# Performance work log

Hardware: AMD Instinct MI355X
Metric: run time of the kernel (lower is better)

## Reference

```python
import jax, jax.numpy as jnp
import numpy as np

B, S, C, H = 8, 1024, 512, 8
DH = C // H  # channels per head


def setup_inputs() -> dict:
    key = jax.random.key(0)
    ks = jax.random.split(key, 10)
    s = 1.0 / np.sqrt(C)
    return {
        "pe_lin_encoding": jax.random.normal(ks[0], (B, S, C), jnp.float32),
        "pe_lin_skip": jax.random.normal(ks[1], (B, S, C), jnp.float32),
        "Wq": jax.random.normal(ks[2], (C, C), jnp.float32) * s,
        "bq": jax.random.normal(ks[3], (C,), jnp.float32) * s,
        "Wk": jax.random.normal(ks[4], (C, C), jnp.float32) * s,
        "bk": jax.random.normal(ks[5], (C,), jnp.float32) * s,
        "Wv": jax.random.normal(ks[6], (C, C), jnp.float32) * s,
        "bv": jax.random.normal(ks[7], (C,), jnp.float32) * s,
        "Wo": jax.random.normal(ks[8], (C, C), jnp.float32) * s,
        "bo": jax.random.normal(ks[9], (C,), jnp.float32) * s,
    }


def reference(pe_lin_encoding, pe_lin_skip, Wq, bq, Wk, bk, Wv, bv, Wo, bo):
    # flatten trailing dims (already [B, S, C] here)
    x = pe_lin_encoding.reshape(pe_lin_encoding.shape[0], pe_lin_encoding.shape[1], -1)
    # torch Linear convention: y = x @ W^T + b, W is [out, in]
    q = jnp.einsum("bsc,oc->bso", x, Wq) + bq
    k = jnp.einsum("bsc,oc->bso", x, Wk) + bk
    v = jnp.einsum("bsc,oc->bso", x, Wv) + bv
    # split heads: [B, S, H, DH] -> attention per head
    q = q.reshape(B, S, H, DH)
    k = k.reshape(B, S, H, DH)
    v = v.reshape(B, S, H, DH)
    scale = 1.0 / np.sqrt(DH)
    scores = jnp.einsum("bqhd,bkhd->bhqk", q, k) * scale  # [B,H,S,S]
    attn = jax.nn.softmax(scores, axis=-1)
    ctx = jnp.einsum("bhqk,bkhd->bqhd", attn, v).reshape(B, S, C)
    out = jnp.einsum("bsc,oc->bso", ctx, Wo) + bo
    return out + pe_lin_skip
```

## Files before the change

### kernel.cpp

```cpp
#include <hip/hip_runtime.h>
#include <hip/hip_bf16.h>

typedef unsigned short u16;
typedef unsigned int u32;

constexpr int B  = 8;
constexpr int S  = 1024;
constexpr int C  = 512;
constexpr int H  = 8;
constexpr int DH = 64;
constexpr int M  = B * S;

typedef __attribute__((ext_vector_type(8))) short bf16x8;
typedef __attribute__((ext_vector_type(4))) float f32x4;

#define GLOBAL_AS __attribute__((address_space(1)))
#define LDS_AS    __attribute__((address_space(3)))

#define QSCALE 0.1803368867f

__device__ __forceinline__ float bf2f(u16 u) {
    return __uint_as_float(((u32)u) << 16);
}
__device__ __forceinline__ u16 f2bf(float f) {
    u32 u = __float_as_uint(f);
    u += 0x7fffu + ((u >> 16) & 1u);
    return (u16)(u >> 16);
}
__device__ __forceinline__ u32 pack2(float a, float b) {
    return (u32)f2bf(a) | ((u32)f2bf(b) << 16);
}
__device__ __forceinline__ void async_cp16(const u16* g, u16* l) {
    __builtin_amdgcn_global_load_lds((const GLOBAL_AS void*)g, (LDS_AS void*)l, 16, 0, 0);
}

constexpr int NX4 = M * C / 4;
constexpr int NW4 = C * C / 4;

__global__ __launch_bounds__(256) void cvt_kernel(
    const float* __restrict__ x,
    const float* __restrict__ wq, const float* __restrict__ wk,
    const float* __restrict__ wv, const float* __restrict__ wo,
    u16* __restrict__ xb, u16* __restrict__ wqkv, u16* __restrict__ wob)
{
    const int i = blockIdx.x * 256 + threadIdx.x;
    const float* src; u16* dst; int off;
    if      (i < NX4)          { src = x;  dst = xb;           off = i; }
    else if (i < NX4 +   NW4)  { src = wq; dst = wqkv;         off = i - NX4; }
    else if (i < NX4 + 2*NW4)  { src = wk; dst = wqkv + C*C;   off = i - NX4 -   NW4; }
    else if (i < NX4 + 3*NW4)  { src = wv; dst = wqkv + 2*C*C; off = i - NX4 - 2*NW4; }
    else                       { src = wo; dst = wob;          off = i - NX4 - 3*NW4; }
    float4 v = ((const float4*)src)[off];
    uint2 p; p.x = pack2(v.x, v.y); p.y = pack2(v.z, v.w);
    ((uint2*)dst)[off] = p;
}

__global__ __launch_bounds__(256) void qkv_gemm(
    const u16* __restrict__ xb, const u16* __restrict__ wqkv,
    const float* __restrict__ bq, const float* __restrict__ bk,
    const float* __restrict__ bv,
    u16* __restrict__ Qo, u16* __restrict__ Ko, u16* __restrict__ Vo)
{
    __shared__ alignas(16) u16 smem[128 * 136];
    u16* const Asm = smem;
    u16* const Bsm = smem + 128 * 64;

    const int mTile = blockIdx.x * 128;
    const int nTile = blockIdx.y * 128;
    const int t = threadIdx.x, lane = t & 63, w = t >> 6;
    const int ql = lane & 15, quad = lane >> 4;
    const int wm = (w & 1) * 64, wn = (w >> 1) * 64;

    f32x4 acc[4][4];
    #pragma unroll
    for (int i = 0; i < 4; i++)
        #pragma unroll
        for (int j = 0; j < 4; j++) acc[i][j] = (f32x4){0.f, 0.f, 0.f, 0.f};

    for (int k0 = 0; k0 < C; k0 += 64) {
        __syncthreads();
        #pragma unroll
        for (int q = 0; q < 4; q++) {
            const int chunk = q * 256 + t;
            const int row = chunk >> 3, c8 = (chunk & 7) * 8;
            async_cp16(xb   + (size_t)(mTile + row) * C + k0 + c8, &Asm[row * 64 + c8]);
            async_cp16(wqkv + (size_t)(nTile + row) * C + k0 + c8, &Bsm[row * 64 + c8]);
        }
        __syncthreads();

        #pragma unroll
        for (int ks = 0; ks < 64; ks += 32) {
            bf16x8 af[4], bfr[4];
            #pragma unroll
            for (int i = 0; i < 4; i++)
                af[i] = *(const bf16x8*)&Asm[(wm + i*16 + ql) * 64 + ks + quad*8];
            #pragma unroll
            for (int j = 0; j < 4; j++)
                bfr[j] = *(const bf16x8*)&Bsm[(wn + j*16 + ql) * 64 + ks + quad*8];
            #pragma unroll
            for (int i = 0; i < 4; i++)
                #pragma unroll
                for (int j = 0; j < 4; j++)
                    acc[i][j] = __builtin_amdgcn_mfma_f32_16x16x32_bf16(af[i], bfr[j], acc[i][j], 0, 0, 0);
        }
    }

    const int z = nTile >> 9;
    const int nBase = nTile & 511;
    if (z == 2) {
        __syncthreads();
        u16* const T = smem;
        #pragma unroll
        for (int j = 0; j < 4; j++) {
            const int n = wn + j*16 + ql;
            const float bj = bv[nBase + n];
            #pragma unroll
            for (int i = 0; i < 4; i++)
                #pragma unroll
                for (int r = 0; r < 4; r++)
                    T[n * 136 + wm + i*16 + quad*4 + r] = f2bf(acc[i][j][r] + bj);
        }
        __syncthreads();
        const int bb = mTile >> 10, ssBase = mTile & 1023;
        #pragma unroll
        for (int q = 0; q < 8; q++) {
            const int c = q * 256 + t;
            const int row = c >> 4, col = (c & 15) * 8;
            const int o = nBase + row, h = o >> 6, d = o & 63;
            *(float4*)(Vo + ((size_t)((bb*H + h) * DH + d)) * S + ssBase + col) =
                *(const float4*)&T[row * 136 + col];
        }
    } else {
        const float* bias = (z == 0) ? bq : bk;
        u16* dst          = (z == 0) ? Qo : Ko;
        const float sc    = (z == 0) ? QSCALE : 1.0f;
        #pragma unroll
        for (int j = 0; j < 4; j++) {
            const int o = nBase + wn + j*16 + ql;
            const float bj = bias[o];
            const int h = o >> 6, d = o & 63;
            #pragma unroll
            for (int i = 0; i < 4; i++) {
                #pragma unroll
                for (int r = 0; r < 4; r++) {
                    const int m = mTile + wm + i*16 + quad*4 + r;
                    const int bb = m >> 10, ss = m & 1023;
                    dst[(size_t)((bb*H + h) * S + ss) * DH + d] = f2bf((acc[i][j][r] + bj) * sc);
                }
            }
        }
    }
}

__global__ __launch_bounds__(256) void attn_kernel(
    const u16* __restrict__ Qo,
    const u16* __restrict__ Ko,
    const u16* __restrict__ Vo,
    u16* __restrict__ ctx)
{
    __shared__ alignas(16) u16 KsU[64 * 64];
    __shared__ alignas(16) u16 VsU[64 * 64];
    __shared__ alignas(16) u16 Ps [64 * 72];

    const int g = blockIdx.x;
    const int xcd = g & 7, slot = g >> 3;
    const int bh = xcd * 8 + (slot >> 4);
    const int qt = slot & 15;

    const int t = threadIdx.x;
    const int lane = t & 63, w = t >> 6;
    const int ql = lane & 15, quad = lane >> 4;

    const u16* Qb = Qo + (size_t)bh * S * DH;
    const u16* Kb = Ko + (size_t)bh * S * DH;
    const u16* Vt = Vo + (size_t)bh * DH * S;

    const int qrow = qt*64 + w*16 + ql;
    const bf16x8 qf0 = *(const bf16x8*)(Qb + (size_t)qrow * DH + quad*8);
    const bf16x8 qf1 = *(const bf16x8*)(Qb + (size_t)qrow * DH + 32 + quad*8);

    bf16x8 onesf;
    #pragma unroll
    for (int i = 0; i < 8; i++) onesf[i] = (short)0x3F80;

    const int swzA = ((quad       ^ (ql & 7)) << 3);
    const int swzB = (((quad + 4) ^ (ql & 7)) << 3);

    f32x4 acc[4], accl;
    #pragma unroll
    for (int dt = 0; dt < 4; dt++) acc[dt] = (f32x4){0.f, 0.f, 0.f, 0.f};
    accl = (f32x4){0.f, 0.f, 0.f, 0.f};

    for (int k0 = 0; k0 < S; k0 += 64) {
        __syncthreads();
        #pragma unroll
        for (int q = 0; q < 2; q++) {
            const int idx = q * 256 + t;
            const int row = idx >> 3, cc = idx & 7;
            const int scol = ((cc ^ (row & 7)) << 3);
            float4 kv = *(const float4*)(Kb + (size_t)(k0 + row) * DH + cc*8);
            float4 vv = *(const float4*)(Vt + (size_t)row * S + k0 + cc*8);
            *(float4*)&KsU[row * 64 + scol] = kv;
            *(float4*)&VsU[row * 64 + scol] = vv;
        }
        __syncthreads();

        f32x4 sc[4];
        #pragma unroll
        for (int nt = 0; nt < 4; nt++) {
            sc[nt] = (f32x4){0.f, 0.f, 0.f, 0.f};
            const bf16x8 kf0 = *(const bf16x8*)&KsU[(nt*16 + ql) * 64 + swzA];
            const bf16x8 kf1 = *(const bf16x8*)&KsU[(nt*16 + ql) * 64 + swzB];
            sc[nt] = __builtin_amdgcn_mfma_f32_16x16x32_bf16(qf0, kf0, sc[nt], 0, 0, 0);
            sc[nt] = __builtin_amdgcn_mfma_f32_16x16x32_bf16(qf1, kf1, sc[nt], 0, 0, 0);
        }

        #pragma unroll
        for (int r = 0; r < 4; r++) {
            const int prow = w*16 + quad*4 + r;
            Ps[prow * 72 +  0 + ql] = f2bf(exp2f(sc[0][r]));
            Ps[prow * 72 + 16 + ql] = f2bf(exp2f(sc[1][r]));
            Ps[prow * 72 + 32 + ql] = f2bf(exp2f(sc[2][r]));
            Ps[prow * 72 + 48 + ql] = f2bf(exp2f(sc[3][r]));
        }

        #pragma unroll
        for (int c = 0; c < 2; c++) {
            const bf16x8 pf = *(const bf16x8*)&Ps[(w*16 + ql) * 72 + c*32 + quad*8];
            const int swz = (c == 0) ? swzA : swzB;
            #pragma unroll
            for (int dt = 0; dt < 4; dt++) {
                const bf16x8 vf = *(const bf16x8*)&VsU[(dt*16 + ql) * 64 + swz];
                acc[dt] = __builtin_amdgcn_mfma_f32_16x16x32_bf16(pf, vf, acc[dt], 0, 0, 0);
            }
            accl = __builtin_amdgcn_mfma_f32_16x16x32_bf16(pf, onesf, accl, 0, 0, 0);
        }
    }

    const int b_ = bh >> 3, h = bh & 7;
    #pragma unroll
    for (int r = 0; r < 4; r++) {
        const float inv = 1.0f / accl[r];
        const int srow = qt*64 + w*16 + quad*4 + r;
        const size_t base = ((size_t)(b_*S + srow)) * C + h*DH;
        #pragma unroll
        for (int dt = 0; dt < 4; dt++)
            ctx[base + dt*16 + ql] = f2bf(acc[dt][r] * inv);
    }
}

__global__ __launch_bounds__(256) void out_gemm(
    const u16* __restrict__ ctx, const u16* __restrict__ wob,
    const float* __restrict__ bo, const float* __restrict__ skip,
    float* __restrict__ out)
{
    __shared__ alignas(16) u16 Asm[128 * 64];
    __shared__ alignas(16) u16 Bsm[128 * 64];

    const int mTile = blockIdx.x * 128;
    const int nTile = blockIdx.y * 128;
    const int t = threadIdx.x, lane = t & 63, w = t >> 6;
    const int ql = lane & 15, quad = lane >> 4;
    const int wm = (w & 1) * 64, wn = (w >> 1) * 64;

    f32x4 acc[4][4];
    #pragma unroll
    for (int i = 0; i < 4; i++)
        #pragma unroll
        for (int j = 0; j < 4; j++) acc[i][j] = (f32x4){0.f, 0.f, 0.f, 0.f};

    for (int k0 = 0; k0 < C; k0 += 64) {
        __syncthreads();
        #pragma unroll
        for (int q = 0; q < 4; q++) {
            const int chunk = q * 256 + t;
            const int row = chunk >> 3, c8 = (chunk & 7) * 8;
            async_cp16(ctx + (size_t)(mTile + row) * C + k0 + c8, &Asm[row * 64 + c8]);
            async_cp16(wob + (size_t)(nTile + row) * C + k0 + c8, &Bsm[row * 64 + c8]);
        }
        __syncthreads();

        #pragma unroll
        for (int ks = 0; ks < 64; ks += 32) {
            bf16x8 af[4], bfr[4];
            #pragma unroll
            for (int i = 0; i < 4; i++)
                af[i] = *(const bf16x8*)&Asm[(wm + i*16 + ql) * 64 + ks + quad*8];
            #pragma unroll
            for (int j = 0; j < 4; j++)
                bfr[j] = *(const bf16x8*)&Bsm[(wn + j*16 + ql) * 64 + ks + quad*8];
            #pragma unroll
            for (int i = 0; i < 4; i++)
                #pragma unroll
                for (int j = 0; j < 4; j++)
                    acc[i][j] = __builtin_amdgcn_mfma_f32_16x16x32_bf16(af[i], bfr[j], acc[i][j], 0, 0, 0);
        }
    }

    #pragma unroll
    for (int j = 0; j < 4; j++) {
        const int o = nTile + wn + j*16 + ql;
        const float bj = bo[o];
        #pragma unroll
        for (int i = 0; i < 4; i++) {
            #pragma unroll
            for (int r = 0; r < 4; r++) {
                const int m = mTile + wm + i*16 + quad*4 + r;
                const size_t idx = (size_t)m * C + o;
                out[idx] = acc[i][j][r] + bj + skip[idx];
            }
        }
    }
}

extern "C" void kernel_launch(void* const* d_in, const int* in_sizes, int n_in,
                              void* d_out, int out_size, void* d_ws, size_t ws_size,
                              hipStream_t stream) {
    (void)in_sizes; (void)n_in; (void)out_size; (void)ws_size;
    const float* x    = (const float*)d_in[0];
    const float* skip = (const float*)d_in[1];
    const float* Wq   = (const float*)d_in[2];
    const float* bq   = (const float*)d_in[3];
    const float* Wk   = (const float*)d_in[4];
    const float* bk   = (const float*)d_in[5];
    const float* Wv   = (const float*)d_in[6];
    const float* bv   = (const float*)d_in[7];
    const float* Wo   = (const float*)d_in[8];
    const float* bo   = (const float*)d_in[9];
    float* out = (float*)d_out;

    u16* xb   = (u16*)d_ws;
    u16* wqkv = xb   + (size_t)M * C;
    u16* wob  = wqkv + (size_t)3 * C * C;
    u16* Qo   = wob  + (size_t)C * C;
    u16* Ko   = Qo   + (size_t)B * H * S * DH;
    u16* Vo   = Ko   + (size_t)B * H * S * DH;
    u16* ctx  = xb;

    cvt_kernel<<<dim3((NX4 + 4 * NW4) / 256), 256, 0, stream>>>(
        x, Wq, Wk, Wv, Wo, xb, wqkv, wob);
    qkv_gemm<<<dim3(M / 128, 1536 / 128), 256, 0, stream>>>(
        xb, wqkv, bq, bk, bv, Qo, Ko, Vo);
    attn_kernel<<<dim3(1024), 256, 0, stream>>>(Qo, Ko, Vo, ctx);
    out_gemm<<<dim3(M / 128, C / 128), 256, 0, stream>>>(
        ctx, wob, bo, skip, out);
}
```

Baseline: 179.2 us.

## Rework attention to 32x32 MFMA with register P and double-buffered K/V

Rewrites the attention kernel to use 32x32x16 MFMAs computing S^T = K·Q^T, so the exp'd probabilities stay in registers. They are packed with v_cvt_pk_bf16 and rearranged with v_permlane32_swap instead of going through an LDS round trip. K/V tiles are double-buffered in LDS with register prefetch of the next tile, which drops one barrier per iteration. Each block now handles 128 query rows with half the grid. This cuts LDS traffic and synchronisation, at the cost of higher register pressure and fewer blocks.

```diff
diff --git a/kernel.cpp b/kernel.cpp
--- a/kernel.cpp
+++ b/kernel.cpp
@@ -13,6 +13,8 @@
 
 typedef __attribute__((ext_vector_type(8))) short bf16x8;
 typedef __attribute__((ext_vector_type(4))) float f32x4;
+typedef __attribute__((ext_vector_type(16))) float f32x16;
+typedef __attribute__((ext_vector_type(4))) u32 u32x4;
 
 #define GLOBAL_AS __attribute__((address_space(1)))
 #define LDS_AS    __attribute__((address_space(3)))
@@ -30,8 +32,19 @@
 __device__ __forceinline__ u32 pack2(float a, float b) {
     return (u32)f2bf(a) | ((u32)f2bf(b) << 16);
 }
+__device__ __forceinline__ u32 cvtpk(float a, float b) {
+    u32 d;
+    asm("v_cvt_pk_bf16_f32 %0, %1, %2" : "=v"(d) : "v"(a), "v"(b));
+    return d;
+}
 __device__ __forceinline__ void async_cp16(const u16* g, u16* l) {
     __builtin_amdgcn_global_load_lds((const GLOBAL_AS void*)g, (LDS_AS void*)l, 16, 0, 0);
+}
+__device__ __forceinline__ f32x16 zero16() {
+    f32x16 z;
+    #pragma unroll
+    for (int i = 0; i < 16; i++) z[i] = 0.f;
+    return z;
 }
 
 constexpr int NX4 = M * C / 4;
@@ -158,94 +171,106 @@
     const u16* __restrict__ Vo,
     u16* __restrict__ ctx)
 {
-    __shared__ alignas(16) u16 KsU[64 * 64];
-    __shared__ alignas(16) u16 VsU[64 * 64];
-    __shared__ alignas(16) u16 Ps [64 * 72];
+    __shared__ alignas(16) u16 KV[2][2][64 * 64];
 
     const int g = blockIdx.x;
     const int xcd = g & 7, slot = g >> 3;
-    const int bh = xcd * 8 + (slot >> 4);
-    const int qt = slot & 15;
+    const int bh = xcd * 8 + (slot >> 3);
+    const int qt = slot & 7;
 
     const int t = threadIdx.x;
     const int lane = t & 63, w = t >> 6;
-    const int ql = lane & 15, quad = lane >> 4;
-
-    const u16* Qb = Qo + (size_t)bh * S * DH;
-    const u16* Kb = Ko + (size_t)bh * S * DH;
-    const u16* Vt = Vo + (size_t)bh * DH * S;
-
-    const int qrow = qt*64 + w*16 + ql;
-    const bf16x8 qf0 = *(const bf16x8*)(Qb + (size_t)qrow * DH + quad*8);
-    const bf16x8 qf1 = *(const bf16x8*)(Qb + (size_t)qrow * DH + 32 + quad*8);
+    const int l31 = lane & 31, hi = lane >> 5;
+    const int sxh8 = ((l31 & 7) ^ hi) << 3;
+    const int kRow = l31 * 64;
+
+    const u16* __restrict__ Qb = Qo + (size_t)bh * S * DH;
+    const u16* __restrict__ Kb = Ko + (size_t)bh * S * DH;
+    const u16* __restrict__ Vt = Vo + (size_t)bh * DH * S;
+
+    const int qrow = qt * 128 + w * 32 + l31;
+    bf16x8 qf[4];
+    #pragma unroll
+    for (int ks = 0; ks < 4; ks++)
+        qf[ks] = *(const bf16x8*)(Qb + (size_t)qrow * DH + ks * 16 + hi * 8);
 
     bf16x8 onesf;
     #pragma unroll
     for (int i = 0; i < 8; i++) onesf[i] = (short)0x3F80;
 
-    const int swzA = ((quad       ^ (ql & 7)) << 3);
-    const int swzB = (((quad + 4) ^ (ql & 7)) << 3);
-
-    f32x4 acc[4], accl;
-    #pragma unroll
-    for (int dt = 0; dt < 4; dt++) acc[dt] = (f32x4){0.f, 0.f, 0.f, 0.f};
-    accl = (f32x4){0.f, 0.f, 0.f, 0.f};
-
+    f32x16 acc[2], accl;
+    acc[0] = zero16(); acc[1] = zero16(); accl = zero16();
+
+    float4 kreg[2], vreg[2];
+    const int srow0 = t >> 3, scc = t & 7;
+    const int scol = ((scc ^ (srow0 & 7)) << 3);
+
+    auto LOADT = [&](int k0) {
+        #pragma unroll
+        for (int q2 = 0; q2 < 2; q2++) {
+            const int row = q2 * 32 + srow0;
+            kreg[q2] = *(const float4*)(Kb + (size_t)(k0 + row) * DH + scc * 8);
+            vreg[q2] = *(const float4*)(Vt + (size_t)row * S + k0 + scc * 8);
+        }
+    };
+    auto STORET = [&](int buf) {
+        #pragma unroll
+        for (int q2 = 0; q2 < 2; q2++) {
+            const int row = q2 * 32 + srow0;
+            *(float4*)&KV[buf][0][row * 64 + scol] = kreg[q2];
+            *(float4*)&KV[buf][1][row * 64 + scol] = vreg[q2];
+        }
+    };
+
+    LOADT(0);
+    #pragma unroll 2
     for (int k0 = 0; k0 < S; k0 += 64) {
-        __syncthreads();
-        #pragma unroll
-        for (int q = 0; q < 2; q++) {
-            const int idx = q * 256 + t;
-            const int row = idx >> 3, cc = idx & 7;
-            const int scol = ((cc ^ (row & 7)) << 3);
-            float4 kv = *(const float4*)(Kb + (size_t)(k0 + row) * DH + cc*8);
-            float4 vv = *(const float4*)(Vt + (size_t)row * S + k0 + cc*8);
-            *(float4*)&KsU[row * 64 + scol] = kv;
-            *(float4*)&VsU[row * 64 + scol] = vv;
-        }
-        __syncthreads();
-
-        f32x4 sc[4];
-        #pragma unroll
-        for (int nt = 0; nt < 4; nt++) {
-            sc[nt] = (f32x4){0.f, 0.f, 0.f, 0.f};
-            const bf16x8 kf0 = *(const bf16x8*)&KsU[(nt*16 + ql) * 64 + swzA];
-            const bf16x8 kf1 = *(const bf16x8*)&KsU[(nt*16 + ql) * 64 + swzB];
-            sc[nt] = __builtin_amdgcn_mfma_f32_16x16x32_bf16(qf0, kf0, sc[nt], 0, 0, 0);
-            sc[nt] = __builtin_amdgcn_mfma_f32_16x16x32_bf16(qf1, kf1, sc[nt], 0, 0, 0);
-        }
-
-        #pragma unroll
-        for (int r = 0; r < 4; r++) {
-            const int prow = w*16 + quad*4 + r;
-            Ps[prow * 72 +  0 + ql] = f2bf(exp2f(sc[0][r]));
-            Ps[prow * 72 + 16 + ql] = f2bf(exp2f(sc[1][r]));
-            Ps[prow * 72 + 32 + ql] = f2bf(exp2f(sc[2][r]));
-            Ps[prow * 72 + 48 + ql] = f2bf(exp2f(sc[3][r]));
-        }
-
-        #pragma unroll
-        for (int c = 0; c < 2; c++) {
-            const bf16x8 pf = *(const bf16x8*)&Ps[(w*16 + ql) * 72 + c*32 + quad*8];
-            const int swz = (c == 0) ? swzA : swzB;
-            #pragma unroll
-            for (int dt = 0; dt < 4; dt++) {
-                const bf16x8 vf = *(const bf16x8*)&VsU[(dt*16 + ql) * 64 + swz];
-                acc[dt] = __builtin_amdgcn_mfma_f32_16x16x32_bf16(pf, vf, acc[dt], 0, 0, 0);
+        const int buf = (k0 >> 6) & 1;
+        STORET(buf);
+        __syncthreads();
+        if (k0 + 64 < S) LOADT(k0 + 64);
+        const u16* Ks = KV[buf][0];
+        const u16* Vs = KV[buf][1];
+
+        #pragma unroll
+        for (int kt = 0; kt < 2; kt++) {
+            f32x16 sc = zero16();
+            #pragma unroll
+            for (int ks = 0; ks < 4; ks++) {
+                const bf16x8 kf = *(const bf16x8*)&Ks[kRow + kt * 2048 + ((ks << 4) ^ sxh8)];
+                sc = __builtin_amdgcn_mfma_f32_32x32x16_bf16(kf, qf[ks], sc, 0, 0, 0);
             }
-            accl = __builtin_amdgcn_mfma_f32_16x16x32_bf16(pf, onesf, accl, 0, 0, 0);
+            #pragma unroll
+            for (int s = 0; s < 2; s++) {
+                u32 x0 = cvtpk(exp2f(sc[8*s+0]), exp2f(sc[8*s+1]));
+                u32 x1 = cvtpk(exp2f(sc[8*s+2]), exp2f(sc[8*s+3]));
+                u32 y0 = cvtpk(exp2f(sc[8*s+4]), exp2f(sc[8*s+5]));
+                u32 y1 = cvtpk(exp2f(sc[8*s+6]), exp2f(sc[8*s+7]));
+                asm("v_permlane32_swap_b32 %0, %1" : "+v"(x0), "+v"(y0));
+                asm("v_permlane32_swap_b32 %0, %1" : "+v"(x1), "+v"(y1));
+                u32x4 pw; pw.x = x0; pw.y = x1; pw.z = y0; pw.w = y1;
+                const bf16x8 pa = __builtin_bit_cast(bf16x8, pw);
+
+                const int ccol = (((kt * 4 + s * 2) << 3) ^ sxh8);
+                #pragma unroll
+                for (int nt = 0; nt < 2; nt++) {
+                    const bf16x8 vf = *(const bf16x8*)&Vs[kRow + nt * 2048 + ccol];
+                    acc[nt] = __builtin_amdgcn_mfma_f32_32x32x16_bf16(pa, vf, acc[nt], 0, 0, 0);
+                }
+                accl = __builtin_amdgcn_mfma_f32_32x32x16_bf16(pa, onesf, accl, 0, 0, 0);
+            }
         }
     }
 
     const int b_ = bh >> 3, h = bh & 7;
-    #pragma unroll
-    for (int r = 0; r < 4; r++) {
+    const int qbase2 = qt * 128 + w * 32 + 4 * hi;
+    #pragma unroll
+    for (int r = 0; r < 16; r++) {
         const float inv = 1.0f / accl[r];
-        const int srow = qt*64 + w*16 + quad*4 + r;
-        const size_t base = ((size_t)(b_*S + srow)) * C + h*DH;
-        #pragma unroll
-        for (int dt = 0; dt < 4; dt++)
-            ctx[base + dt*16 + ql] = f2bf(acc[dt][r] * inv);
+        const int srow = qbase2 + (r & 3) + 8 * (r >> 2);
+        const size_t base = ((size_t)(b_ * S + srow)) * C + h * DH + l31;
+        ctx[base]      = f2bf(acc[0][r] * inv);
+        ctx[base + 32] = f2bf(acc[1][r] * inv);
     }
 }
 
@@ -341,7 +366,7 @@
         x, Wq, Wk, Wv, Wo, xb, wqkv, wob);
     qkv_gemm<<<dim3(M / 128, 1536 / 128), 256, 0, stream>>>(
         xb, wqkv, bq, bk, bv, Qo, Ko, Vo);
-    attn_kernel<<<dim3(1024), 256, 0, stream>>>(Qo, Ko, Vo, ctx);
+    attn_kernel<<<dim3(512), 256, 0, stream>>>(Qo, Ko, Vo, ctx);
     out_gemm<<<dim3(M / 128, C / 128), 256, 0, stream>>>(
         ctx, wob, bo, skip, out);
 }
```

After: 196.9 us. 1.1x slower.
